# Optimization experiments

Hardware: AMD Instinct MI355X
Metric: run time of the kernel (lower is better)

The kernel has to match this reference:

```python
import jax, jax.numpy as jnp
import numpy as np

B, C, U = 8, 32, 32
K = 5            # powers = k + 1 with k = 4
N1, N2 = 256, 256


def setup_inputs() -> dict:
    key = jax.random.key(0)
    k_x, k_c1, k_c2, k_w = jax.random.split(key, 4)
    x = jax.random.normal(k_x, (B, C, N1, N2), dtype=jnp.float32)
    # Chebyshev polynomial bases T_0..T_k of the (rescaled) Laplacians of the
    # two factor graphs; registered buffers in the torch module.
    cheb1 = jax.random.normal(k_c1, (K, N1, N1), dtype=jnp.float32)
    cheb2 = jax.random.normal(k_c2, (K, N2, N2), dtype=jnp.float32)
    # Trainable anisotropic coefficients [powers, powers, channels, units],
    # initialized N(0, 0.001) in the original module.
    coefs = jax.random.normal(k_w, (K, K, C, U), dtype=jnp.float32) * 0.001
    return {"x": x, "cheb1": cheb1, "cheb2": cheb2, "coefs": coefs}


def reference(x, cheb1, cheb2, coefs):
    """Fused form of the anisotropic Chebyshev convolution.

    Original triple loop computes
      out[b,u,m,n] = sum_{k1,k2,i,p,q}
          coefs[k1,k2,i,u] * cheb1[k1,p,m] * cheb2[k2,q,n] * x[b,i,p,q]
    """
    # Filter along the first graph axis for every power k1: [B, K, C, N1, N2]
    a = jnp.einsum('kpm,bipq->bkimq', cheb1, x)
    # Contract channels and k1 with the learned coefficients: [B, K, U, N1, N2]
    c = jnp.einsum('bkimq,kliu->blumq', a, coefs)
    # Filter along the second graph axis for every power k2: [B, U, N1, N2]
    out = jnp.einsum('blumq,lqn->bumn', c, cheb2)
    return out
```

## Files before the change

### kernel.cpp

```cpp
#include <hip/hip_runtime.h>
#include <stdint.h>

#define WB 8
#define WC 32
#define WU 32
#define WK 5
#define WN 256
#define NN 65536
#define KC 160
#define KQ 1280

typedef __attribute__((ext_vector_type(8))) short bf8;
typedef __attribute__((ext_vector_type(8))) unsigned short us8;
typedef __attribute__((ext_vector_type(4))) float f4;

__device__ __forceinline__ unsigned short f2b(float f) {
    union { float f; uint32_t u; } v; v.f = f;
    uint32_t u = v.u;
    return (unsigned short)((u + 0x7FFFu + ((u >> 16) & 1u)) >> 16);
}

__device__ __forceinline__ void gload16(const unsigned short* g, unsigned short* l) {
    __builtin_amdgcn_global_load_lds(
        (const __attribute__((address_space(1))) unsigned int*)g,
        (__attribute__((address_space(3))) unsigned int*)l, 16, 0, 0);
}

__global__ void prep_small(const float* __restrict__ cheb1,
                           const float* __restrict__ cheb2,
                           const float* __restrict__ coefs,
                           unsigned short* __restrict__ c1T,
                           unsigned short* __restrict__ c2T,
                           unsigned short* __restrict__ Wt) {
    int idx = blockIdx.x * 256 + threadIdx.x;
    if (idx < WK * NN) {
        int k = idx / NN, r = idx % NN, m = r / WN, p = r % WN;
        c1T[idx] = f2b(cheb1[(k * WN + p) * WN + m]);
    }
    if (idx < WN * KQ) {
        int n = idx / KQ, r = idx % KQ;
        c2T[idx] = f2b(cheb2[r * WN + n]);
    }
    if (idx < KC * KC) {
        int lu = idx / KC, ki = idx % KC;
        int l = lu >> 5, u = lu & 31, k = ki >> 5, i = ki & 31;
        Wt[idx] = f2b(coefs[((k * WK + l) * WC + i) * WU + u]);
    }
}

__global__ void prep_x(const float* __restrict__ x, unsigned short* __restrict__ xT) {
    __shared__ unsigned short tile[64][72];
    int bi = blockIdx.z;
    int p0 = blockIdx.y * 64, q0 = blockIdx.x * 64;
    const float* src = x + (size_t)bi * NN;
    unsigned short* dst = xT + (size_t)bi * NN;
    int t = threadIdx.x;
    int c4 = (t & 15) * 4, r0 = t >> 4;
    for (int it = 0; it < 4; ++it) {
        int r = r0 + it * 16;
        float4 v = *reinterpret_cast<const float4*>(&src[(size_t)(p0 + r) * WN + q0 + c4]);
        tile[r][c4 + 0] = f2b(v.x); tile[r][c4 + 1] = f2b(v.y);
        tile[r][c4 + 2] = f2b(v.z); tile[r][c4 + 3] = f2b(v.w);
    }
    __syncthreads();
    for (int it = 0; it < 4; ++it) {
        int q = r0 + it * 16;
        ushort4 o;
        o.x = tile[c4 + 0][q]; o.y = tile[c4 + 1][q];
        o.z = tile[c4 + 2][q]; o.w = tile[c4 + 3][q];
        *reinterpret_cast<ushort4*>(&dst[(size_t)(q0 + q) * WN + p0 + c4]) = o;
    }
}

__global__ __launch_bounds__(512, 4) void g1(const unsigned short* __restrict__ c1T,
                                             const unsigned short* __restrict__ xT,
                                             unsigned short* __restrict__ a, int b_base) {
    __shared__ unsigned short As[2][128 * 64];
    __shared__ unsigned short Bs[256 * 64];
    int p = blockIdx.x;
    int gpx = gridDim.x / 80;
    int xcd = p & 7, j = p >> 3;
    int grp = xcd * gpx + j / 10;
    int member = j % 10;
    int bl = grp >> 5, i = grp & 31;
    int row0 = member * 128;
    int b = b_base + bl;
    const unsigned short* Asrc = c1T;
    const unsigned short* Bsrc = xT + (size_t)(b * WC + i) * NN;
    unsigned short* Out = a + (size_t)bl * KC * NN;

    int t = threadIdx.x;
    int w = t >> 6, l = t & 63;
    int wm = (w >> 2) * 64, wn = (w & 3) * 64;
    int lr = l & 15, hi = l >> 4;
    int srow = l >> 3;
    int scol = ((l & 7) ^ srow) * 8;

    f4 acc[4][4];
    for (int mf = 0; mf < 4; ++mf) for (int nf = 0; nf < 4; ++nf) acc[mf][nf] = (f4)(0.0f);

#define G1_STAGE_A(buf, step) do { \
    int p0_ = (step) * 64; \
    for (int it = 0; it < 2; ++it) { \
        int chunk = it * 8 + w; int row = chunk * 8 + srow; \
        gload16(&Asrc[(size_t)(row0 + row) * 256 + p0_ + scol], &As[buf][chunk * 512]); } \
} while (0)
#define G1_STAGE_B(step) do { \
    int p0_ = (step) * 64; \
    for (int it = 0; it < 4; ++it) { \
        int chunk = it * 8 + w; int row = chunk * 8 + srow; \
        gload16(&Bsrc[(size_t)row * 256 + p0_ + scol], &Bs[chunk * 512]); } \
} while (0)

    G1_STAGE_A(0, 0);
    for (int step = 0; step < 4; ++step) {
        int cur = step & 1;
        G1_STAGE_B(step);
        if (step < 3) {
            G1_STAGE_A(cur ^ 1, step + 1);
            asm volatile("s_waitcnt vmcnt(2)" ::: "memory");
        } else {
            asm volatile("s_waitcnt vmcnt(0)" ::: "memory");
        }
        __builtin_amdgcn_s_barrier();
        asm volatile("" ::: "memory");
        for (int kk = 0; kk < 2; ++kk) {
            bf8 af[4], bfr[4];
            for (int mf = 0; mf < 4; ++mf) {
                int r = wm + mf * 16 + lr;
                af[mf] = *(const bf8*)&As[cur][r * 64 + (((kk * 4 + hi) ^ (r & 7)) * 8)];
            }
            for (int nf = 0; nf < 4; ++nf) {
                int rb = wn + nf * 16 + lr;
                bfr[nf] = *(const bf8*)&Bs[rb * 64 + (((kk * 4 + hi) ^ (rb & 7)) * 8)];
            }
            for (int mf = 0; mf < 4; ++mf)
                for (int nf = 0; nf < 4; ++nf)
                    acc[mf][nf] = __builtin_amdgcn_mfma_f32_16x16x32_bf16(af[mf], bfr[nf], acc[mf][nf], 0, 0, 0);
        }
        asm volatile("" ::: "memory");
        __builtin_amdgcn_s_barrier();
    }
#undef G1_STAGE_A
#undef G1_STAGE_B
    for (int mf = 0; mf < 4; ++mf)
        for (int nf = 0; nf < 4; ++nf)
            for (int j2 = 0; j2 < 4; ++j2) {
                int grow = row0 + wm + mf * 16 + hi * 4 + j2;
                int k = grow >> 8, m = grow & 255;
                int q = wn + nf * 16 + lr;
                Out[(size_t)(k * 32 + i) * NN + m * 256 + q] = f2b(acc[mf][nf][j2]);
            }
}

__global__ __launch_bounds__(512, 4) void g2p(const unsigned short* __restrict__ Wt,
                                              const unsigned short* __restrict__ a,
                                              unsigned short* __restrict__ c) {
    __shared__ unsigned short Bt[128 * 172];
    int bl = blockIdx.y;
    int n0 = blockIdx.x * 128;
    const unsigned short* asrc = a + (size_t)bl * KC * NN;
    unsigned short* Out = c + (size_t)bl * KC * NN;
    int t = threadIdx.x;

    for (int s = 0; s < 2; ++s) {
        int task = t + s * 512;
        if (task < 640) {
            int oct = task & 15, kq = task >> 4;
            const unsigned short* src = asrc + (size_t)(kq * 4) * NN + n0 + oct * 8;
            us8 v0 = *(const us8*)&src[0 * NN];
            us8 v1 = *(const us8*)&src[1 * NN];
            us8 v2 = *(const us8*)&src[2 * NN];
            us8 v3 = *(const us8*)&src[3 * NN];
            #pragma unroll
            for (int j = 0; j < 8; ++j) {
                ushort4 wv;
                wv.x = v0[j]; wv.y = v1[j]; wv.z = v2[j]; wv.w = v3[j];
                *reinterpret_cast<ushort4*>(&Bt[(oct * 8 + j) * 172 + kq * 4]) = wv;
            }
        }
    }
    __syncthreads();

    int w = t >> 6, l = t & 63;
    int mh = w >> 2, nq = w & 3;
    int lr = l & 15, hi = l >> 4;
    f4 acc[5][2];
    for (int mf = 0; mf < 5; ++mf) { acc[mf][0] = (f4)(0.0f); acc[mf][1] = (f4)(0.0f); }

    for (int kk = 0; kk < 5; ++kk) {
        int k0 = kk * 32 + hi * 8;
        bf8 bfr[2];
        #pragma unroll
        for (int nf = 0; nf < 2; ++nf) {
            int pix = (nq * 2 + nf) * 16 + lr;
            typedef __attribute__((ext_vector_type(4))) short s4v;
            s4v lo  = *(const s4v*)&Bt[pix * 172 + k0];
            s4v hi4 = *(const s4v*)&Bt[pix * 172 + k0 + 4];
            bfr[nf] = __builtin_shufflevector(lo, hi4, 0, 1, 2, 3, 4, 5, 6, 7);
        }
        #pragma unroll
        for (int mf = 0; mf < 5; ++mf) {
            int row = mh * 80 + mf * 16 + lr;
            bf8 afr = *(const bf8*)&Wt[(size_t)row * KC + k0];
            acc[mf][0] = __builtin_amdgcn_mfma_f32_16x16x32_bf16(afr, bfr[0], acc[mf][0], 0, 0, 0);
            acc[mf][1] = __builtin_amdgcn_mfma_f32_16x16x32_bf16(afr, bfr[1], acc[mf][1], 0, 0, 0);
        }
    }
    for (int mf = 0; mf < 5; ++mf)
        for (int nf = 0; nf < 2; ++nf)
            for (int j = 0; j < 4; ++j) {
                int row = mh * 80 + mf * 16 + hi * 4 + j;
                int col = n0 + (nq * 2 + nf) * 16 + lr;
                Out[(size_t)row * NN + col] = f2b(acc[mf][nf][j]);
            }
}

__global__ __launch_bounds__(512, 4) void g3(const unsigned short* __restrict__ c,
                                             const unsigned short* __restrict__ c2T,
                                             float* __restrict__ out, int b_base) {
    __shared__ unsigned short As[2][128 * 64];
    __shared__ unsigned short Bs[256 * 64];
    int bl = blockIdx.y;
    int b = b_base + bl;
    int R0 = blockIdx.x * 128;
    int u = R0 >> 8, m0 = R0 & 255;
    const unsigned short* Csrc = c + (size_t)bl * KC * NN;

    int t = threadIdx.x;
    int w = t >> 6, l = t & 63;
    int wm = (w >> 2) * 64, wn = (w & 3) * 64;
    int lr = l & 15, hi = l >> 4;
    int srow = l >> 3;
    int scol = ((l & 7) ^ srow) * 8;

    f4 acc[4][4];
    for (int mf = 0; mf < 4; ++mf) for (int nf = 0; nf < 4; ++nf) acc[mf][nf] = (f4)(0.0f);

#define G3_STAGE_A(buf, step) do { \
    int lq_ = (step) >> 2, q0_ = ((step) & 3) * 64; \
    const unsigned short* Arow0 = Csrc + (size_t)(lq_ * 32 + u) * NN + (size_t)m0 * 256 + q0_; \
    for (int it = 0; it < 2; ++it) { \
        int chunk = it * 8 + w; int row = chunk * 8 + srow; \
        gload16(&Arow0[(size_t)row * 256 + scol], &As[buf][chunk * 512]); } \
} while (0)
#define G3_STAGE_B(step) do { \
    const unsigned short* Brow0 = c2T + (step) * 64; \
    for (int it = 0; it < 4; ++it) { \
        int chunk = it * 8 + w; int row = chunk * 8 + srow; \
        gload16(&Brow0[(size_t)row * KQ + scol], &Bs[chunk * 512]); } \
} while (0)

    G3_STAGE_A(0, 0);
    for (int step = 0; step < 20; ++step) {
        int cur = step & 1;
        G3_STAGE_B(step);
        if (step < 19) {
            G3_STAGE_A(cur ^ 1, step + 1);
            asm volatile("s_waitcnt vmcnt(2)" ::: "memory");
        } else {
            asm volatile("s_waitcnt vmcnt(0)" ::: "memory");
        }
        __builtin_amdgcn_s_barrier();
        asm volatile("" ::: "memory");
        for (int kk = 0; kk < 2; ++kk) {
            bf8 af[4], bfr[4];
            for (int mf = 0; mf < 4; ++mf) {
                int r = wm + mf * 16 + lr;
                af[mf] = *(const bf8*)&As[cur][r * 64 + (((kk * 4 + hi) ^ (r & 7)) * 8)];
            }
            for (int nf = 0; nf < 4; ++nf) {
                int rb = wn + nf * 16 + lr;
                bfr[nf] = *(const bf8*)&Bs[rb * 64 + (((kk * 4 + hi) ^ (rb & 7)) * 8)];
            }
            for (int mf = 0; mf < 4; ++mf)
                for (int nf = 0; nf < 4; ++nf)
                    acc[mf][nf] = __builtin_amdgcn_mfma_f32_16x16x32_bf16(af[mf], bfr[nf], acc[mf][nf], 0, 0, 0);
        }
        asm volatile("" ::: "memory");
        __builtin_amdgcn_s_barrier();
    }
#undef G3_STAGE_A
#undef G3_STAGE_B
    for (int mf = 0; mf < 4; ++mf)
        for (int nf = 0; nf < 4; ++nf)
            for (int j = 0; j < 4; ++j) {
                int m = m0 + wm + mf * 16 + hi * 4 + j;
                int n = wn + nf * 16 + lr;
                out[((size_t)(b * WU + u) * WN + m) * WN + n] = acc[mf][nf][j];
            }
}

extern "C" void kernel_launch(void* const* d_in, const int* in_sizes, int n_in,
                              void* d_out, int out_size, void* d_ws, size_t ws_size,
                              hipStream_t stream) {
    const float* x     = (const float*)d_in[0];
    const float* cheb1 = (const float*)d_in[1];
    const float* cheb2 = (const float*)d_in[2];
    const float* coefs = (const float*)d_in[3];
    float* out = (float*)d_out;
    unsigned short* ws = (unsigned short*)d_ws;

    size_t off = 0;
    unsigned short* xT  = ws + off; off += (size_t)WB * WC * NN;
    unsigned short* c1T = ws + off; off += (size_t)WK * NN;
    unsigned short* c2T = ws + off; off += (size_t)WN * KQ;
    unsigned short* Wt  = ws + off; off += (size_t)KC * KC;
    size_t fixed_elems = off;
    size_t a1 = (size_t)KC * NN;

    prep_small<<<1280, 256, 0, stream>>>(cheb1, cheb2, coefs, c1T, c2T, Wt);
    prep_x<<<dim3(4, 4, WB * WC), 256, 0, stream>>>(x, xT);

    size_t avail = ws_size / 2;
    size_t rem = avail > fixed_elems ? avail - fixed_elems : 0;

    if (rem >= 9 * a1) {
        int nb = (int)((rem - 8 * a1) / a1);
        if (nb < 1) nb = 1;
        if (nb > WB) nb = WB;
        unsigned short* a_ = ws + fixed_elems;
        unsigned short* c_ = a_ + (size_t)nb * a1;
        for (int b0 = 0; b0 < WB; b0 += nb) {
            int cur = (WB - b0 < nb) ? (WB - b0) : nb;
            g1<<<dim3(cur * 320), 512, 0, stream>>>(c1T, xT, a_, b0);
            g2p<<<dim3(512, cur), 512, 0, stream>>>(Wt, a_, c_ + (size_t)b0 * a1);
        }
        g3<<<dim3(64, WB), 512, 0, stream>>>(c_, c2T, out, 0);
    } else {
        size_t per_b = 2 * a1;
        int nb = (int)(rem / per_b);
        if (nb < 1) nb = 1;
        if (nb > WB) nb = WB;
        unsigned short* a_ = ws + fixed_elems;
        unsigned short* c_ = a_ + (size_t)nb * a1;
        for (int b0 = 0; b0 < WB; b0 += nb) {
            int cur = (WB - b0 < nb) ? (WB - b0) : nb;
            g1<<<dim3(cur * 320), 512, 0, stream>>>(c1T, xT, a_, b0);
            g2p<<<dim3(512, cur), 512, 0, stream>>>(Wt, a_, c_);
            g3<<<dim3(64, cur), 512, 0, stream>>>(c_, c2T, out, b0);
        }
    }
}
```

Measured before the change: 280.4 us.

## Store intermediate in pixel-tiled layout so second GEMM stages via direct LDS loads

```diff
diff --git a/kernel.cpp b/kernel.cpp
--- a/kernel.cpp
+++ b/kernel.cpp
@@ -144,45 +144,32 @@
 #undef G1_STAGE_A
 #undef G1_STAGE_B
     for (int mf = 0; mf < 4; ++mf)
-        for (int nf = 0; nf < 4; ++nf)
+        for (int nf = 0; nf < 4; ++nf) {
+            int qv = wn + nf * 16;
             for (int j2 = 0; j2 < 4; ++j2) {
                 int grow = row0 + wm + mf * 16 + hi * 4 + j2;
                 int k = grow >> 8, m = grow & 255;
-                int q = wn + nf * 16 + lr;
-                Out[(size_t)(k * 32 + i) * NN + m * 256 + q] = f2b(acc[mf][nf][j2]);
-            }
+                int pixg = m * 16 + (qv >> 4);
+                Out[(size_t)pixg * 2560 + (k * 32 + i) * 16 + lr] = f2b(acc[mf][nf][j2]);
+            }
+        }
 }
 
 __global__ __launch_bounds__(512, 4) void g2p(const unsigned short* __restrict__ Wt,
                                               const unsigned short* __restrict__ a,
                                               unsigned short* __restrict__ c) {
-    __shared__ unsigned short Bt[128 * 172];
+    __shared__ unsigned short Bt[20480];
     int bl = blockIdx.y;
     int n0 = blockIdx.x * 128;
-    const unsigned short* asrc = a + (size_t)bl * KC * NN;
+    const unsigned short* asrc = a + (size_t)bl * KC * NN + (size_t)(n0 >> 4) * 2560;
     unsigned short* Out = c + (size_t)bl * KC * NN;
     int t = threadIdx.x;
-
-    for (int s = 0; s < 2; ++s) {
-        int task = t + s * 512;
-        if (task < 640) {
-            int oct = task & 15, kq = task >> 4;
-            const unsigned short* src = asrc + (size_t)(kq * 4) * NN + n0 + oct * 8;
-            us8 v0 = *(const us8*)&src[0 * NN];
-            us8 v1 = *(const us8*)&src[1 * NN];
-            us8 v2 = *(const us8*)&src[2 * NN];
-            us8 v3 = *(const us8*)&src[3 * NN];
-            #pragma unroll
-            for (int j = 0; j < 8; ++j) {
-                ushort4 wv;
-                wv.x = v0[j]; wv.y = v1[j]; wv.z = v2[j]; wv.w = v3[j];
-                *reinterpret_cast<ushort4*>(&Bt[(oct * 8 + j) * 172 + kq * 4]) = wv;
-            }
-        }
-    }
+    int w = t >> 6, l = t & 63;
+
+    for (int s = 0; s < 5; ++s)
+        gload16(&asrc[(size_t)(s * 512 + t) * 8], &Bt[(s * 512 + w * 64) * 8]);
     __syncthreads();
 
-    int w = t >> 6, l = t & 63;
     int mh = w >> 2, nq = w & 3;
     int lr = l & 15, hi = l >> 4;
     f4 acc[5][2];
@@ -193,11 +180,12 @@
         bf8 bfr[2];
         #pragma unroll
         for (int nf = 0; nf < 2; ++nf) {
-            int pix = (nq * 2 + nf) * 16 + lr;
-            typedef __attribute__((ext_vector_type(4))) short s4v;
-            s4v lo  = *(const s4v*)&Bt[pix * 172 + k0];
-            s4v hi4 = *(const s4v*)&Bt[pix * 172 + k0 + 4];
-            bfr[nf] = __builtin_shufflevector(lo, hi4, 0, 1, 2, 3, 4, 5, 6, 7);
+            int base = (nq * 2 + nf) * 2560 + lr;
+            bf8 v;
+            #pragma unroll
+            for (int e = 0; e < 8; ++e)
+                v[e] = (short)Bt[base + (k0 + e) * 16];
+            bfr[nf] = v;
         }
         #pragma unroll
         for (int mf = 0; mf < 5; ++mf) {
```

Result: slower. 290.4 us (+3.6%).
